# Optimization experiments

Hardware: AMD Instinct MI355X
Metric: run time of the kernel (lower is better)

## Reference

```python
import jax, jax.numpy as jnp
import numpy as np

B, N, D, H, E = 4, 1024, 512, 8, 5
HD = D // H  # head_dim = 64


def _xavier(k, shape):
    fan_out, fan_in = shape
    s = (2.0 / (fan_in + fan_out)) ** 0.5
    return jax.random.normal(k, shape, jnp.float32) * s


def setup_inputs() -> dict:
    key = jax.random.key(0)
    ks = jax.random.split(key, 7)
    x = jax.random.normal(ks[0], (B, N, D), jnp.float32)
    edge_features = jax.random.normal(ks[1], (B, N, N, E), jnp.float32)
    node_mask = jax.random.randint(ks[2], (B, N), 0, 2).astype(bool)
    w_qkv = _xavier(ks[3], (3 * D, D))
    w_ep = _xavier(ks[4], (H, E))
    w_eg = _xavier(ks[5], (H, E))
    b_eg = jnp.zeros((H,), jnp.float32)
    w_proj = _xavier(ks[6], (D, D))
    b_proj = jnp.zeros((D,), jnp.float32)
    return {"x": x, "edge_features": edge_features, "node_mask": node_mask,
            "w_qkv": w_qkv, "w_ep": w_ep, "w_eg": w_eg, "b_eg": b_eg,
            "w_proj": w_proj, "b_proj": b_proj}


def reference(x, edge_features, node_mask, w_qkv, w_ep, w_eg, b_eg, w_proj, b_proj):
    b, n, d = x.shape
    scale = HD ** -0.5
    # qkv projection (torch Linear: y = x @ W^T), split into q,k,v (b,H,n,HD)
    qkv = (x @ w_qkv.T).reshape(b, n, 3, H, HD)
    qkv = jnp.transpose(qkv, (2, 0, 3, 1, 4))
    q, k, v = qkv[0], qkv[1], qkv[2]
    # attention scores (b,H,n,n)
    scores = jnp.einsum('bhnd,bhmd->bhnm', q, k) * scale
    # edge bias and sigmoid gate, (b,n,n,E) @ (E,H) -> (b,H,n,n)
    edge_bias = jnp.einsum('bnme,he->bhnm', edge_features, w_ep)
    edge_gates = jax.nn.sigmoid(
        jnp.einsum('bnme,he->bhnm', edge_features, w_eg) + b_eg[None, :, None, None])
    scores = scores + edge_gates * edge_bias
    # pairwise valid mask, broadcast over heads
    m = node_mask[:, None, :, None] & node_mask[:, None, None, :]  # (b,1,n,n)
    scores = jnp.where(m, scores, -jnp.inf)
    row_valid = jnp.any(m, axis=-1)  # (b,1,n)
    scores = jnp.where(row_valid[..., None], scores, 0.0)
    attn = jax.nn.softmax(scores, axis=-1)
    out = jnp.einsum('bhnm,bhmd->bhnd', attn, v)
    out = jnp.transpose(out, (0, 2, 1, 3)).reshape(b, n, d)
    return out @ w_proj.T + b_proj
```

## Files before the change

kernel.cpp:

```cpp
#include <hip/hip_runtime.h>
#include <hip/hip_bf16.h>

#define Bb 4
#define Nn 1024
#define Dd 512
#define Hh 8
#define Ee 5
#define HDd 64

typedef unsigned int u32_t;
typedef unsigned short u16_t;
typedef short s16x8 __attribute__((ext_vector_type(8)));
typedef float f32x4 __attribute__((ext_vector_type(4)));

#define MFMA(a, b, c) __builtin_amdgcn_mfma_f32_16x16x32_bf16((a), (b), (c), 0, 0, 0)

__device__ __forceinline__ void lds_barrier() {
    asm volatile("s_waitcnt lgkmcnt(0)" ::: "memory");
    __builtin_amdgcn_s_barrier();
    asm volatile("" ::: "memory");
}

__device__ __forceinline__ u32_t pack32(float x) {
    u32_t u = __float_as_uint(x);
    u32_t hi = u & 0xffff0000u;
    float rem = x - __uint_as_float(hi);
    u32_t r = __float_as_uint(rem);
    u32_t lo = (r + 0x7fffu + ((r >> 16) & 1u)) >> 16;
    return hi | (lo & 0xffffu);
}

__device__ __forceinline__ void unpk8(uint4 A, uint4 B, s16x8& h, s16x8& l) {
    union { u16_t u[8]; s16x8 v; } H, L;
    u32_t a[8] = {A.x, A.y, A.z, A.w, B.x, B.y, B.z, B.w};
    #pragma unroll
    for (int i = 0; i < 8; i++) { H.u[i] = (u16_t)(a[i] >> 16); L.u[i] = (u16_t)(a[i] & 0xffffu); }
    h = H.v; l = L.v;
}

__device__ __forceinline__ void split4(uint4 A, uint2& hi, uint2& lo) {
    hi.x = (A.x >> 16) | (A.y & 0xffff0000u);
    hi.y = (A.z >> 16) | (A.w & 0xffff0000u);
    lo.x = (A.x & 0xffffu) | (A.y << 16);
    lo.y = (A.z & 0xffffu) | (A.w << 16);
}

__device__ __forceinline__ void stage16(uint4 A0, uint4 A1, uint4 A2, uint4 A3,
                                        u16_t* dh, u16_t* dl) {
    uint2 h0, l0, h1, l1, h2, l2, h3, l3;
    split4(A0, h0, l0); split4(A1, h1, l1); split4(A2, h2, l2); split4(A3, h3, l3);
    *(uint4*)(dh + 0) = make_uint4(h0.x, h0.y, h1.x, h1.y);
    *(uint4*)(dh + 8) = make_uint4(h2.x, h2.y, h3.x, h3.y);
    *(uint4*)(dl + 0) = make_uint4(l0.x, l0.y, l1.x, l1.y);
    *(uint4*)(dl + 8) = make_uint4(l2.x, l2.y, l3.x, l3.y);
}

#define HHW(a, b) (((a) >> 16) | ((b) & 0xffff0000u))
#define LLW(a, b) (((a) & 0xffffu) | ((b) << 16))

__global__ __launch_bounds__(256) void pack_prep(const float* __restrict__ x,
                                                 const float* __restrict__ wq,
                                                 const float* __restrict__ wpj,
                                                 const void* __restrict__ msk,
                                                 u32_t* __restrict__ xp,
                                                 u32_t* __restrict__ wqp,
                                                 u32_t* __restrict__ wpp,
                                                 u32_t* __restrict__ mb,
                                                 int* __restrict__ anyB) {
    __shared__ int notint;
    __shared__ int ab[Bb];
    const int tid = threadIdx.x;
    if (blockIdx.x == 1024) {
        if (tid == 0) notint = 0;
        if (tid < Bb) ab[tid] = 0;
        __syncthreads();
        const u32_t* wp = (const u32_t*)msk;
        int bad = 0;
        for (int i = tid; i < 1024; i += 256) bad |= (wp[i] > 1u);
        if (bad) atomicOr(&notint, 1);
        __syncthreads();
        const int isbyte = notint;
        const unsigned char* bp = (const unsigned char*)msk;
        if (tid < 128) {
            u32_t wbits = 0;
            for (int k = 0; k < 32; k++) {
                const int i = tid * 32 + k;
                const int v = isbyte ? (bp[i] != 0) : (wp[i] != 0);
                wbits |= (u32_t)v << k;
            }
            mb[tid] = wbits;
            if (wbits) atomicOr(&ab[tid >> 5], 1);
        }
        __syncthreads();
        if (tid < Bb) anyB[tid] = ab[tid];
        return;
    }
    const int gt = blockIdx.x * 256 + tid;
    const int gs = 1024 * 256;
    const float4* xs = (const float4*)x;
    uint4* xd = (uint4*)xp;
    for (int i = gt; i < (Bb * Nn * Dd) / 4; i += gs) {
        float4 v = xs[i];
        xd[i] = make_uint4(pack32(v.x), pack32(v.y), pack32(v.z), pack32(v.w));
    }
    const float4* qs = (const float4*)wq;
    uint4* qd = (uint4*)wqp;
    for (int i = gt; i < (3 * Dd * Dd) / 4; i += gs) {
        float4 v = qs[i];
        qd[i] = make_uint4(pack32(v.x), pack32(v.y), pack32(v.z), pack32(v.w));
    }
    const float4* ps = (const float4*)wpj;
    uint4* pd = (uint4*)wpp;
    for (int i = gt; i < (Dd * Dd) / 4; i += gs) {
        float4 v = ps[i];
        pd[i] = make_uint4(pack32(v.x), pack32(v.y), pack32(v.z), pack32(v.w));
    }
}

__global__ __launch_bounds__(256) void qkv_mfma(const u32_t* __restrict__ xp,
                                                const u32_t* __restrict__ wp,
                                                u32_t* __restrict__ q32,
                                                u32_t* __restrict__ k32,
                                                u32_t* __restrict__ v32) {
    __shared__ __align__(16) u16_t Xh[64 * 72], Xl[64 * 72];
    __shared__ __align__(16) u16_t Wh[64 * 72], Wl[64 * 72];
    const int tid = threadIdx.x;
    const int wv = tid >> 6, lane = tid & 63, lm = lane & 15, quad = lane >> 4;
    const int m0 = blockIdx.y * 64, c0 = blockIdx.x * 64;
    const int row = tid >> 2, dq = tid & 3;
    const uint4* x4 = (const uint4*)xp;
    const uint4* w4 = (const uint4*)wp;

    const size_t xb0 = (size_t)(m0 + row) * 128 + dq * 4;
    const size_t wb0 = (size_t)(c0 + row) * 128 + dq * 4;
    uint4 xa0 = x4[xb0 + 0], xa1 = x4[xb0 + 1], xa2 = x4[xb0 + 2], xa3 = x4[xb0 + 3];
    uint4 wa0 = w4[wb0 + 0], wa1 = w4[wb0 + 1], wa2 = w4[wb0 + 2], wa3 = w4[wb0 + 3];

    f32x4 acc[4];
    #pragma unroll
    for (int nt = 0; nt < 4; nt++) acc[nt] = {0.f, 0.f, 0.f, 0.f};

    for (int kt = 0; kt < 8; kt++) {
        lds_barrier();
        stage16(xa0, xa1, xa2, xa3, &Xh[row * 72 + dq * 16], &Xl[row * 72 + dq * 16]);
        stage16(wa0, wa1, wa2, wa3, &Wh[row * 72 + dq * 16], &Wl[row * 72 + dq * 16]);
        const int ktn = (kt < 7) ? kt + 1 : 7;
        xa0 = x4[xb0 + ktn * 16 + 0]; xa1 = x4[xb0 + ktn * 16 + 1];
        xa2 = x4[xb0 + ktn * 16 + 2]; xa3 = x4[xb0 + ktn * 16 + 3];
        wa0 = w4[wb0 + ktn * 16 + 0]; wa1 = w4[wb0 + ktn * 16 + 1];
        wa2 = w4[wb0 + ktn * 16 + 2]; wa3 = w4[wb0 + ktn * 16 + 3];
        lds_barrier();
        s16x8 ah[2], al[2];
        #pragma unroll
        for (int ks = 0; ks < 2; ks++) {
            ah[ks] = *(const s16x8*)&Xh[(16 * wv + lm) * 72 + ks * 32 + quad * 8];
            al[ks] = *(const s16x8*)&Xl[(16 * wv + lm) * 72 + ks * 32 + quad * 8];
        }
        #pragma unroll
        for (int nt = 0; nt < 4; nt++) {
            #pragma unroll
            for (int ks = 0; ks < 2; ks++) {
                s16x8 bh = *(const s16x8*)&Wh[(16 * nt + lm) * 72 + ks * 32 + quad * 8];
                s16x8 bl = *(const s16x8*)&Wl[(16 * nt + lm) * 72 + ks * 32 + quad * 8];
                acc[nt] = MFMA(ah[ks], bh, acc[nt]);
                acc[nt] = MFMA(ah[ks], bl, acc[nt]);
                acc[nt] = MFMA(al[ks], bh, acc[nt]);
            }
        }
    }
    #pragma unroll
    for (int nt = 0; nt < 4; nt++) {
        const int c = c0 + 16 * nt + lm;
        const int s = c >> 9, hd = c & 511, h = hd >> 6, d = hd & 63;
        u32_t* dst = (s == 0) ? q32 : (s == 1) ? k32 : v32;
        #pragma unroll
        for (int r = 0; r < 4; r++) {
            const int m = m0 + 16 * wv + 4 * quad + r;
            const int b = m >> 10, n = m & (Nn - 1);
            dst[(((size_t)b * Hh + h) * Nn + n) * HDd + d] = pack32(acc[nt][r]);
        }
    }
}

__global__ __launch_bounds__(256, 2) void attn_mfma(const u32_t* __restrict__ q32,
                                                    const u32_t* __restrict__ k32,
                                                    const u32_t* __restrict__ v32,
                                                    const float* __restrict__ ef,
                                                    const u32_t* __restrict__ mb,
                                                    const int* __restrict__ anyB,
                                                    const float* __restrict__ wep,
                                                    const float* __restrict__ weg,
                                                    const float* __restrict__ beg,
                                                    u32_t* __restrict__ aoutp) {
    __shared__ __align__(16) u16_t Kh[64 * 72], Kl[64 * 72];
    __shared__ __align__(16) u16_t VTh[64 * 88], VTl[64 * 88];
    __shared__ __align__(16) u32_t Ppk[64 * 68];

    const int tid = threadIdx.x;
    const int wv = tid >> 6, lane = tid & 63, lm = lane & 15, quad = lane >> 4;
    const int i0 = blockIdx.x * 64;
    const int h  = blockIdx.y;
    const int b  = blockIdx.z;
    const int row = tid >> 2, dq = tid & 3;
    const int jo = tid >> 5, dch = tid & 31;

    const uint4* kg4 = (const uint4*)(k32 + (((size_t)b * Hh + h) * Nn) * HDd);
    const uint2* vg2 = (const uint2*)(v32 + (((size_t)b * Hh + h) * Nn) * HDd);
    const u32_t* mbB = mb + b * 32;

    const int i_sm = i0 + 16 * wv + lm;

    const u32_t* qrow = q32 + (((size_t)b * Hh + h) * Nn + i_sm) * HDd;
    uint4 qA0 = *(const uint4*)&qrow[quad * 8];
    uint4 qB0 = *(const uint4*)&qrow[quad * 8 + 4];
    uint4 qA1 = *(const uint4*)&qrow[32 + quad * 8];
    uint4 qB1 = *(const uint4*)&qrow[32 + quad * 8 + 4];
    const size_t kb0 = (size_t)row * 16 + dq * 4;
    uint4 kr0 = kg4[kb0 + 0], kr1 = kg4[kb0 + 1], kr2 = kg4[kb0 + 2], kr3 = kg4[kb0 + 3];
    uint2 vq0 = vg2[(8 * jo + 0) * 32 + dch], vq1 = vg2[(8 * jo + 1) * 32 + dch],
          vq2 = vg2[(8 * jo + 2) * 32 + dch], vq3 = vg2[(8 * jo + 3) * 32 + dch],
          vq4 = vg2[(8 * jo + 4) * 32 + dch], vq5 = vg2[(8 * jo + 5) * 32 + dch],
          vq6 = vg2[(8 * jo + 6) * 32 + dch], vq7 = vg2[(8 * jo + 7) * 32 + dch];

    const float* efL = ef + ((size_t)(b * Nn + i_sm) * Nn + 4 * quad) * Ee;
    uint2 mwc = *(const uint2*)&mbB[0];
    float4 er4[4][5];
    #pragma unroll
    for (int jn = 0; jn < 4; jn++) {
        const float4* p4 = (const float4*)(efL + (size_t)(16 * jn) * Ee);
        #pragma unroll
        for (int c = 0; c < 5; c++) er4[jn][c] = p4[c];
    }

    const float wp0 = wep[h*Ee+0], wp1 = wep[h*Ee+1], wp2 = wep[h*Ee+2],
                wp3 = wep[h*Ee+3], wp4 = wep[h*Ee+4];
    const float wg0 = weg[h*Ee+0], wg1 = weg[h*Ee+1], wg2 = weg[h*Ee+2],
                wg3 = weg[h*Ee+3], wg4 = weg[h*Ee+4];
    const float bgs = beg[h];
    const int anyb = anyB[b];
    const int rvs = anyb && ((mbB[i_sm >> 5] >> (i_sm & 31)) & 1);

    s16x8 qh[2], ql[2];
    unpk8(qA0, qB0, qh[0], ql[0]);
    unpk8(qA1, qB1, qh[1], ql[1]);

    float m_ = -1e30f, l_ = 0.f;
    f32x4 accO[4];
    #pragma unroll
    for (int dn = 0; dn < 4; dn++) accO[dn] = {0.f, 0.f, 0.f, 0.f};
    const int xk = 8 * (lm & 3);

    for (int jt = 0; jt < Nn / 64; jt++) {
        const int jtn = (jt + 1 < Nn / 64) ? jt + 1 : Nn / 64 - 1;
        const int j0n = jtn * 64;

        lds_barrier();

        stage16(kr0, kr1, kr2, kr3, &Kh[row * 72 + dq * 16], &Kl[row * 72 + dq * 16]);
        {
            const int d0 = 2 * dch, d1 = d0 + 1;
            uint4 H0 = make_uint4(HHW(vq0.x, vq1.x), HHW(vq2.x, vq3.x),
                                  HHW(vq4.x, vq5.x), HHW(vq6.x, vq7.x));
            uint4 L0 = make_uint4(LLW(vq0.x, vq1.x), LLW(vq2.x, vq3.x),
                                  LLW(vq4.x, vq5.x), LLW(vq6.x, vq7.x));
            uint4 H1 = make_uint4(HHW(vq0.y, vq1.y), HHW(vq2.y, vq3.y),
                                  HHW(vq4.y, vq5.y), HHW(vq6.y, vq7.y));
            uint4 L1 = make_uint4(LLW(vq0.y, vq1.y), LLW(vq2.y, vq3.y),
                                  LLW(vq4.y, vq5.y), LLW(vq6.y, vq7.y));
            *(uint4*)&VTh[d0 * 88 + 8 * jo] = H0;
            *(uint4*)&VTl[d0 * 88 + 8 * jo] = L0;
            *(uint4*)&VTh[d1 * 88 + 8 * jo] = H1;
            *(uint4*)&VTl[d1 * 88 + 8 * jo] = L1;
        }
        {
            const size_t kbn = (size_t)(j0n + row) * 16 + dq * 4;
            kr0 = kg4[kbn + 0]; kr1 = kg4[kbn + 1]; kr2 = kg4[kbn + 2]; kr3 = kg4[kbn + 3];
            vq0 = vg2[(j0n + 8 * jo + 0) * 32 + dch];
            vq1 = vg2[(j0n + 8 * jo + 1) * 32 + dch];
            vq2 = vg2[(j0n + 8 * jo + 2) * 32 + dch];
            vq3 = vg2[(j0n + 8 * jo + 3) * 32 + dch];
            vq4 = vg2[(j0n + 8 * jo + 4) * 32 + dch];
            vq5 = vg2[(j0n + 8 * jo + 5) * 32 + dch];
            vq6 = vg2[(j0n + 8 * jo + 6) * 32 + dch];
            vq7 = vg2[(j0n + 8 * jo + 7) * 32 + dch];
        }

        lds_barrier();

        f32x4 Sp[4];
        #pragma unroll
        for (int jn = 0; jn < 4; jn++) {
            f32x4 s = {0.f, 0.f, 0.f, 0.f};
            #pragma unroll
            for (int ks = 0; ks < 2; ks++) {
                s16x8 kh = *(const s16x8*)&Kh[(16 * jn + lm) * 72 + ks * 32 + quad * 8];
                s16x8 kl = *(const s16x8*)&Kl[(16 * jn + lm) * 72 + ks * 32 + quad * 8];
                s = MFMA(kh, qh[ks], s);
                s = MFMA(kh, ql[ks], s);
                s = MFMA(kl, qh[ks], s);
            }
            Sp[jn] = s;
        }

        const u32_t sj0 = mwc.x >> (4 * quad), sj1 = mwc.x >> (4 * quad + 16);
        const u32_t sj2 = mwc.y >> (4 * quad), sj3 = mwc.y >> (4 * quad + 16);
        const u32_t sj[4] = {sj0, sj1, sj2, sj3};
        float pp[4][4];
        #pragma unroll
        for (int jn = 0; jn < 4; jn++) {
            #pragma unroll
            for (int r = 0; r < 4; r++) {
                const int mjv = (sj[jn] >> r) & 1;
                const int f = r * 5;
                const float e0 = er4[jn][(f+0)>>2][(f+0)&3];
                const float e1 = er4[jn][(f+1)>>2][(f+1)&3];
                const float e2 = er4[jn][(f+2)>>2][(f+2)&3];
                const float e3 = er4[jn][(f+3)>>2][(f+3)&3];
                const float e4 = er4[jn][(f+4)>>2][(f+4)&3];
                const float bias = fmaf(e0, wp0, fmaf(e1, wp1, fmaf(e2, wp2, fmaf(e3, wp3, e4 * wp4))));
                const float gv = fmaf(e0, wg0, fmaf(e1, wg1, fmaf(e2, wg2, fmaf(e3, wg3, fmaf(e4, wg4, bgs)))));
                const float gate = __builtin_amdgcn_rcpf(1.f + __expf(-gv));
                const float val = fmaf(Sp[jn][r], 0.125f, gate * bias);
                pp[jn][r] = rvs ? (mjv ? val : -1e30f) : 0.f;
            }
        }
        mwc = *(const uint2*)&mbB[j0n >> 5];
        #pragma unroll
        for (int jn = 0; jn < 4; jn++) {
            const float4* p4 = (const float4*)(efL + (size_t)(j0n + 16 * jn) * Ee);
            #pragma unroll
            for (int c = 0; c < 5; c++) er4[jn][c] = p4[c];
        }

        float tmax = fmaxf(fmaxf(fmaxf(pp[0][0], pp[0][1]), fmaxf(pp[0][2], pp[0][3])),
                           fmaxf(fmaxf(pp[1][0], pp[1][1]), fmaxf(pp[1][2], pp[1][3])));
        tmax = fmaxf(tmax,
               fmaxf(fmaxf(fmaxf(pp[2][0], pp[2][1]), fmaxf(pp[2][2], pp[2][3])),
                     fmaxf(fmaxf(pp[3][0], pp[3][1]), fmaxf(pp[3][2], pp[3][3]))));
        tmax = fmaxf(tmax, __shfl_xor(tmax, 16));
        tmax = fmaxf(tmax, __shfl_xor(tmax, 32));
        const float mnew = fmaxf(m_, tmax);
        const float alpha = __expf(m_ - mnew);
        float ps = 0.f;
        #pragma unroll
        for (int jn = 0; jn < 4; jn++)
            #pragma unroll
            for (int r = 0; r < 4; r++) { pp[jn][r] = __expf(pp[jn][r] - mnew); ps += pp[jn][r]; }
        ps += __shfl_xor(ps, 16);
        ps += __shfl_xor(ps, 32);
        m_ = mnew;
        l_ = l_ * alpha + ps;
        float a4[4];
        #pragma unroll
        for (int r = 0; r < 4; r++) a4[r] = __shfl(alpha, 4 * quad + r);
        #pragma unroll
        for (int dn = 0; dn < 4; dn++)
            #pragma unroll
            for (int r = 0; r < 4; r++) accO[dn][r] *= a4[r];

        #pragma unroll
        for (int jn = 0; jn < 4; jn++) {
            #pragma unroll
            for (int p = 0; p < 2; p++) {
                const int col = (16 * jn + 4 * quad + 2 * p) ^ xk;
                *(uint2*)&Ppk[(16 * wv + lm) * 68 + col] =
                    make_uint2(pack32(pp[jn][2 * p]), pack32(pp[jn][2 * p + 1]));
            }
        }

        s16x8 ph[2], pl[2];
        #pragma unroll
        for (int ks2 = 0; ks2 < 2; ks2++) {
            const int off = (16 * wv + lm) * 68 + ((ks2 * 32 + quad * 8) ^ xk);
            uint4 A = *(const uint4*)&Ppk[off];
            uint4 B2 = *(const uint4*)&Ppk[off + 4];
            unpk8(A, B2, ph[ks2], pl[ks2]);
        }
        #pragma unroll
        for (int dn = 0; dn < 4; dn++) {
            f32x4 c = accO[dn];
            #pragma unroll
            for (int ks2 = 0; ks2 < 2; ks2++) {
                s16x8 vh = *(const s16x8*)&VTh[(16 * dn + lm) * 88 + ks2 * 32 + quad * 8];
                s16x8 vl = *(const s16x8*)&VTl[(16 * dn + lm) * 88 + ks2 * 32 + quad * 8];
                c = MFMA(ph[ks2], vh, c);
                c = MFMA(ph[ks2], vl, c);
                c = MFMA(pl[ks2], vh, c);
            }
            accO[dn] = c;
        }
    }

    float linv[4];
    #pragma unroll
    for (int r = 0; r < 4; r++) linv[r] = __builtin_amdgcn_rcpf(__shfl(l_, 4 * quad + r));
    #pragma unroll
    for (int r = 0; r < 4; r++) {
        const int i = i0 + 16 * wv + 4 * quad + r;
        #pragma unroll
        for (int dn = 0; dn < 4; dn++)
            aoutp[(size_t)(b * Nn + i) * Dd + h * HDd + 16 * dn + lm] = pack32(accO[dn][r] * linv[r]);
    }
}

__global__ __launch_bounds__(256) void out_mfma(const u32_t* __restrict__ ap,
                                                const u32_t* __restrict__ wp,
                                                const float* __restrict__ bias,
                                                float* __restrict__ out) {
    __shared__ __align__(16) u16_t Xh[64 * 72], Xl[64 * 72];
    __shared__ __align__(16) u16_t Wh[64 * 72], Wl[64 * 72];
    const int tid = threadIdx.x;
    const int wv = tid >> 6, lane = tid & 63, lm = lane & 15, quad = lane >> 4;
    const int m0 = blockIdx.y * 64, c0 = blockIdx.x * 64;
    const int row = tid >> 2, dq = tid & 3;
    const uint4* a4 = (const uint4*)ap;
    const uint4* w4 = (const uint4*)wp;

    const size_t ab0 = (size_t)(m0 + row) * 128 + dq * 4;
    const size_t wb0 = (size_t)(c0 + row) * 128 + dq * 4;
    uint4 xa0 = a4[ab0 + 0], xa1 = a4[ab0 + 1], xa2 = a4[ab0 + 2], xa3 = a4[ab0 + 3];
    uint4 wa0 = w4[wb0 + 0], wa1 = w4[wb0 + 1], wa2 = w4[wb0 + 2], wa3 = w4[wb0 + 3];

    f32x4 acc[4];
    #pragma unroll
    for (int nt = 0; nt < 4; nt++) acc[nt] = {0.f, 0.f, 0.f, 0.f};

    for (int kt = 0; kt < 8; kt++) {
        lds_barrier();
        stage16(xa0, xa1, xa2, xa3, &Xh[row * 72 + dq * 16], &Xl[row * 72 + dq * 16]);
        stage16(wa0, wa1, wa2, wa3, &Wh[row * 72 + dq * 16], &Wl[row * 72 + dq * 16]);
        const int ktn = (kt < 7) ? kt + 1 : 7;
        xa0 = a4[ab0 + ktn * 16 + 0]; xa1 = a4[ab0 + ktn * 16 + 1];
        xa2 = a4[ab0 + ktn * 16 + 2]; xa3 = a4[ab0 + ktn * 16 + 3];
        wa0 = w4[wb0 + ktn * 16 + 0]; wa1 = w4[wb0 + ktn * 16 + 1];
        wa2 = w4[wb0 + ktn * 16 + 2]; wa3 = w4[wb0 + ktn * 16 + 3];
        lds_barrier();
        s16x8 ah[2], al[2];
        #pragma unroll
        for (int ks = 0; ks < 2; ks++) {
            ah[ks] = *(const s16x8*)&Xh[(16 * wv + lm) * 72 + ks * 32 + quad * 8];
            al[ks] = *(const s16x8*)&Xl[(16 * wv + lm) * 72 + ks * 32 + quad * 8];
        }
        #pragma unroll
        for (int nt = 0; nt < 4; nt++) {
            #pragma unroll
            for (int ks = 0; ks < 2; ks++) {
                s16x8 bh = *(const s16x8*)&Wh[(16 * nt + lm) * 72 + ks * 32 + quad * 8];
                s16x8 bl = *(const s16x8*)&Wl[(16 * nt + lm) * 72 + ks * 32 + quad * 8];
                acc[nt] = MFMA(ah[ks], bh, acc[nt]);
                acc[nt] = MFMA(ah[ks], bl, acc[nt]);
                acc[nt] = MFMA(al[ks], bh, acc[nt]);
            }
        }
    }
    #pragma unroll
    for (int nt = 0; nt < 4; nt++) {
        const int c = c0 + 16 * nt + lm;
        const float bc = bias[c];
        #pragma unroll
        for (int r = 0; r < 4; r++) {
            const int m = m0 + 16 * wv + 4 * quad + r;
            out[(size_t)m * Dd + c] = acc[nt][r] + bc;
        }
    }
}

extern "C" void kernel_launch(void* const* d_in, const int* in_sizes, int n_in,
                              void* d_out, int out_size, void* d_ws, size_t ws_size,
                              hipStream_t stream) {
    const float* x    = (const float*)d_in[0];
    const float* ef   = (const float*)d_in[1];
    const void*  msk  = d_in[2];
    const float* wqkv = (const float*)d_in[3];
    const float* wep  = (const float*)d_in[4];
    const float* weg  = (const float*)d_in[5];
    const float* beg  = (const float*)d_in[6];
    const float* wpj  = (const float*)d_in[7];
    const float* bpj  = (const float*)d_in[8];
    float* out = (float*)d_out;

    u32_t* mbits = (u32_t*)d_ws;
    int* anyB = (int*)(mbits + 128);
    u32_t* q32 = (u32_t*)(anyB + 16);
    const size_t per = (size_t)Bb * Hh * Nn * HDd;
    u32_t* k32 = q32 + per;
    u32_t* v32 = k32 + per;
    u32_t* aop = v32 + per;
    u32_t* xp  = aop + (size_t)Bb * Nn * Dd;
    u32_t* wqp = xp + (size_t)Bb * Nn * Dd;
    u32_t* wpp = wqp + (size_t)3 * Dd * Dd;

    pack_prep<<<1025, 256, 0, stream>>>(x, wqkv, wpj, msk, xp, wqp, wpp, mbits, anyB);
    qkv_mfma<<<dim3(24, 64), 256, 0, stream>>>(xp, wqp, q32, k32, v32);
    attn_mfma<<<dim3(Nn / 64, Hh, Bb), 256, 0, stream>>>(q32, k32, v32, ef, mbits, anyB,
                                                         wep, weg, beg, aop);
    out_mfma<<<dim3(8, 64), 256, 0, stream>>>(aop, wpp, bpj, out);
}
```

Before: 300.1 us.

## Split attention over key halves with combine kernel and register-shuffled P operand

Splits the attention key range into two halves per query tile, doubling the grid, and adds a combine kernel that merges the partial outputs using the saved row max and sum. The P matrix now stays in registers and is rearranged with cross-lane shuffles, replacing the LDS round trip. The MFMA operand order is swapped so the output is transposed, and the V tile uses XOR swizzling with a narrower LDS pitch. Occupancy is raised to 4 blocks per CU. The cost is an extra kernel launch, extra partial-result memory traffic, and reuse of the xp buffer for partial output.

```diff
diff --git a/kernel.cpp b/kernel.cpp
--- a/kernel.cpp
+++ b/kernel.cpp
@@ -28,6 +28,10 @@
     u32_t r = __float_as_uint(rem);
     u32_t lo = (r + 0x7fffu + ((r >> 16) & 1u)) >> 16;
     return hi | (lo & 0xffffu);
+}
+
+__device__ __forceinline__ float unpkf(u32_t x) {
+    return __uint_as_float(x & 0xffff0000u) + __uint_as_float(x << 16);
 }
 
 __device__ __forceinline__ void unpk8(uint4 A, uint4 B, s16x8& h, s16x8& l) {
@@ -182,7 +186,7 @@
     }
 }
 
-__global__ __launch_bounds__(256, 2) void attn_mfma(const u32_t* __restrict__ q32,
+__global__ __launch_bounds__(256, 4) void attn_mfma(const u32_t* __restrict__ q32,
                                                     const u32_t* __restrict__ k32,
                                                     const u32_t* __restrict__ v32,
                                                     const float* __restrict__ ef,
@@ -191,18 +195,24 @@
                                                     const float* __restrict__ wep,
                                                     const float* __restrict__ weg,
                                                     const float* __restrict__ beg,
-                                                    u32_t* __restrict__ aoutp) {
+                                                    u32_t* __restrict__ pout0,
+                                                    u32_t* __restrict__ pout1,
+                                                    float2* __restrict__ ml0,
+                                                    float2* __restrict__ ml1) {
     __shared__ __align__(16) u16_t Kh[64 * 72], Kl[64 * 72];
-    __shared__ __align__(16) u16_t VTh[64 * 88], VTl[64 * 88];
-    __shared__ __align__(16) u32_t Ppk[64 * 68];
+    __shared__ __align__(16) u16_t VTh[64 * 72], VTl[64 * 72];
 
     const int tid = threadIdx.x;
     const int wv = tid >> 6, lane = tid & 63, lm = lane & 15, quad = lane >> 4;
-    const int i0 = blockIdx.x * 64;
+    const int i0 = (blockIdx.x & 15) * 64;
+    const int half = blockIdx.x >> 4;
+    const int jbase = half * 512;
     const int h  = blockIdx.y;
     const int b  = blockIdx.z;
     const int row = tid >> 2, dq = tid & 3;
     const int jo = tid >> 5, dch = tid & 31;
+    const int wsw = 8 * ((dch >> 2) & 1);
+    const int vsw = 8 * ((lm >> 3) & 1);
 
     const uint4* kg4 = (const uint4*)(k32 + (((size_t)b * Hh + h) * Nn) * HDd);
     const uint2* vg2 = (const uint2*)(v32 + (((size_t)b * Hh + h) * Nn) * HDd);
@@ -215,19 +225,19 @@
     uint4 qB0 = *(const uint4*)&qrow[quad * 8 + 4];
     uint4 qA1 = *(const uint4*)&qrow[32 + quad * 8];
     uint4 qB1 = *(const uint4*)&qrow[32 + quad * 8 + 4];
-    const size_t kb0 = (size_t)row * 16 + dq * 4;
+    const size_t kb0 = (size_t)(jbase + row) * 16 + dq * 4;
     uint4 kr0 = kg4[kb0 + 0], kr1 = kg4[kb0 + 1], kr2 = kg4[kb0 + 2], kr3 = kg4[kb0 + 3];
-    uint2 vq0 = vg2[(8 * jo + 0) * 32 + dch], vq1 = vg2[(8 * jo + 1) * 32 + dch],
-          vq2 = vg2[(8 * jo + 2) * 32 + dch], vq3 = vg2[(8 * jo + 3) * 32 + dch],
-          vq4 = vg2[(8 * jo + 4) * 32 + dch], vq5 = vg2[(8 * jo + 5) * 32 + dch],
-          vq6 = vg2[(8 * jo + 6) * 32 + dch], vq7 = vg2[(8 * jo + 7) * 32 + dch];
+    uint2 vq0 = vg2[(jbase + 8 * jo + 0) * 32 + dch], vq1 = vg2[(jbase + 8 * jo + 1) * 32 + dch],
+          vq2 = vg2[(jbase + 8 * jo + 2) * 32 + dch], vq3 = vg2[(jbase + 8 * jo + 3) * 32 + dch],
+          vq4 = vg2[(jbase + 8 * jo + 4) * 32 + dch], vq5 = vg2[(jbase + 8 * jo + 5) * 32 + dch],
+          vq6 = vg2[(jbase + 8 * jo + 6) * 32 + dch], vq7 = vg2[(jbase + 8 * jo + 7) * 32 + dch];
 
     const float* efL = ef + ((size_t)(b * Nn + i_sm) * Nn + 4 * quad) * Ee;
-    uint2 mwc = *(const uint2*)&mbB[0];
+    uint2 mwc = *(const uint2*)&mbB[jbase >> 5];
     float4 er4[4][5];
     #pragma unroll
     for (int jn = 0; jn < 4; jn++) {
-        const float4* p4 = (const float4*)(efL + (size_t)(16 * jn) * Ee);
+        const float4* p4 = (const float4*)(efL + (size_t)(jbase + 16 * jn) * Ee);
         #pragma unroll
         for (int c = 0; c < 5; c++) er4[jn][c] = p4[c];
     }
@@ -248,17 +258,16 @@
     f32x4 accO[4];
     #pragma unroll
     for (int dn = 0; dn < 4; dn++) accO[dn] = {0.f, 0.f, 0.f, 0.f};
-    const int xk = 8 * (lm & 3);
-
-    for (int jt = 0; jt < Nn / 64; jt++) {
-        const int jtn = (jt + 1 < Nn / 64) ? jt + 1 : Nn / 64 - 1;
-        const int j0n = jtn * 64;
+
+    for (int jt = 0; jt < 8; jt++) {
+        const int j0n = jbase + ((jt < 7) ? jt + 1 : 7) * 64;
 
         lds_barrier();
 
         stage16(kr0, kr1, kr2, kr3, &Kh[row * 72 + dq * 16], &Kl[row * 72 + dq * 16]);
         {
             const int d0 = 2 * dch, d1 = d0 + 1;
+            const int jcol = (8 * jo) ^ wsw;
             uint4 H0 = make_uint4(HHW(vq0.x, vq1.x), HHW(vq2.x, vq3.x),
                                   HHW(vq4.x, vq5.x), HHW(vq6.x, vq7.x));
             uint4 L0 = make_uint4(LLW(vq0.x, vq1.x), LLW(vq2.x, vq3.x),
@@ -267,10 +276,10 @@
                                   HHW(vq4.y, vq5.y), HHW(vq6.y, vq7.y));
             uint4 L1 = make_uint4(LLW(vq0.y, vq1.y), LLW(vq2.y, vq3.y),
                                   LLW(vq4.y, vq5.y), LLW(vq6.y, vq7.y));
-            *(uint4*)&VTh[d0 * 88 + 8 * jo] = H0;
-            *(uint4*)&VTl[d0 * 88 + 8 * jo] = L0;
-            *(uint4*)&VTh[d1 * 88 + 8 * jo] = H1;
-            *(uint4*)&VTl[d1 * 88 + 8 * jo] = L1;
+            *(uint4*)&VTh[d0 * 72 + jcol] = H0;
+            *(uint4*)&VTl[d0 * 72 + jcol] = L0;
+            *(uint4*)&VTh[d1 * 72 + jcol] = H1;
+            *(uint4*)&VTl[d1 * 72 + jcol] = L1;
         }
         {
             const size_t kbn = (size_t)(j0n + row) * 16 + dq * 4;
@@ -302,9 +311,8 @@
             Sp[jn] = s;
         }
 
-        const u32_t sj0 = mwc.x >> (4 * quad), sj1 = mwc.x >> (4 * quad + 16);
-        const u32_t sj2 = mwc.y >> (4 * quad), sj3 = mwc.y >> (4 * quad + 16);
-        const u32_t sj[4] = {sj0, sj1, sj2, sj3};
+        const u32_t sj[4] = {mwc.x >> (4 * quad), mwc.x >> (4 * quad + 16),
+                             mwc.y >> (4 * quad), mwc.y >> (4 * quad + 16)};
         float pp[4][4];
         #pragma unroll
         for (int jn = 0; jn < 4; jn++) {
@@ -350,57 +358,93 @@
         ps += __shfl_xor(ps, 32);
         m_ = mnew;
         l_ = l_ * alpha + ps;
-        float a4[4];
-        #pragma unroll
-        for (int r = 0; r < 4; r++) a4[r] = __shfl(alpha, 4 * quad + r);
-        #pragma unroll
-        for (int dn = 0; dn < 4; dn++)
-            #pragma unroll
-            for (int r = 0; r < 4; r++) accO[dn][r] *= a4[r];
-
-        #pragma unroll
-        for (int jn = 0; jn < 4; jn++) {
-            #pragma unroll
-            for (int p = 0; p < 2; p++) {
-                const int col = (16 * jn + 4 * quad + 2 * p) ^ xk;
-                *(uint2*)&Ppk[(16 * wv + lm) * 68 + col] =
-                    make_uint2(pack32(pp[jn][2 * p]), pack32(pp[jn][2 * p + 1]));
-            }
-        }
-
-        s16x8 ph[2], pl[2];
-        #pragma unroll
-        for (int ks2 = 0; ks2 < 2; ks2++) {
-            const int off = (16 * wv + lm) * 68 + ((ks2 * 32 + quad * 8) ^ xk);
-            uint4 A = *(const uint4*)&Ppk[off];
-            uint4 B2 = *(const uint4*)&Ppk[off + 4];
-            unpk8(A, B2, ph[ks2], pl[ks2]);
-        }
+        #pragma unroll
+        for (int dn = 0; dn < 4; dn++) accO[dn] *= alpha;
+
+        u32_t P32[4][4];
+        #pragma unroll
+        for (int jn = 0; jn < 4; jn++)
+            #pragma unroll
+            for (int r = 0; r < 4; r++) P32[jn][r] = pack32(pp[jn][r]);
+        const bool lowpair = (quad & 2) == 0;
+        u32_t kept[8], send1[8];
+        #pragma unroll
+        for (int t = 0; t < 4; t++) {
+            kept[t]     = lowpair ? P32[0][t] : P32[1][t];
+            kept[4+t]   = lowpair ? P32[2][t] : P32[3][t];
+            send1[t]    = lowpair ? P32[1][t] : P32[0][t];
+            send1[4+t]  = lowpair ? P32[3][t] : P32[2][t];
+        }
+        u32_t R8[8], T8[8];
+        #pragma unroll
+        for (int t = 0; t < 8; t++) R8[t] = __shfl_xor((int)send1[t], 32);
+        const bool sendR = (quad == 0) || (quad == 3);
+        #pragma unroll
+        for (int t = 0; t < 8; t++) {
+            u32_t s2 = sendR ? R8[t] : kept[t];
+            T8[t] = __shfl_xor((int)s2, 16);
+        }
+        u32_t XL[8], XH[8];
+        #pragma unroll
+        for (int t = 0; t < 8; t++) {
+            XL[t] = (quad == 0) ? kept[t] : ((quad == 2) ? R8[t] : T8[t]);
+            XH[t] = (quad == 3) ? kept[t] : ((quad == 1) ? R8[t] : T8[t]);
+        }
+        s16x8 bh[2], bl[2];
+        unpk8(make_uint4(XL[0], XL[1], XL[2], XL[3]),
+              make_uint4(XH[0], XH[1], XH[2], XH[3]), bh[0], bl[0]);
+        unpk8(make_uint4(XL[4], XL[5], XL[6], XL[7]),
+              make_uint4(XH[4], XH[5], XH[6], XH[7]), bh[1], bl[1]);
+
         #pragma unroll
         for (int dn = 0; dn < 4; dn++) {
             f32x4 c = accO[dn];
             #pragma unroll
-            for (int ks2 = 0; ks2 < 2; ks2++) {
-                s16x8 vh = *(const s16x8*)&VTh[(16 * dn + lm) * 88 + ks2 * 32 + quad * 8];
-                s16x8 vl = *(const s16x8*)&VTl[(16 * dn + lm) * 88 + ks2 * 32 + quad * 8];
-                c = MFMA(ph[ks2], vh, c);
-                c = MFMA(ph[ks2], vl, c);
-                c = MFMA(pl[ks2], vh, c);
+            for (int ks = 0; ks < 2; ks++) {
+                const int off = (16 * dn + lm) * 72 + ((ks * 32 + quad * 8) ^ vsw);
+                s16x8 vh = *(const s16x8*)&VTh[off];
+                s16x8 vl = *(const s16x8*)&VTl[off];
+                c = MFMA(vh, bh[ks], c);
+                c = MFMA(vh, bl[ks], c);
+                c = MFMA(vl, bh[ks], c);
             }
             accO[dn] = c;
         }
     }
 
-    float linv[4];
-    #pragma unroll
-    for (int r = 0; r < 4; r++) linv[r] = __builtin_amdgcn_rcpf(__shfl(l_, 4 * quad + r));
-    #pragma unroll
-    for (int r = 0; r < 4; r++) {
-        const int i = i0 + 16 * wv + 4 * quad + r;
-        #pragma unroll
-        for (int dn = 0; dn < 4; dn++)
-            aoutp[(size_t)(b * Nn + i) * Dd + h * HDd + 16 * dn + lm] = pack32(accO[dn][r] * linv[r]);
-    }
+    u32_t* pout = half ? pout1 : pout0;
+    float2* mlo = half ? ml1 : ml0;
+    const size_t obase = (size_t)(b * Nn + i_sm) * Dd + h * HDd;
+    #pragma unroll
+    for (int dn = 0; dn < 4; dn++) {
+        uint4 o = make_uint4(pack32(accO[dn][0]), pack32(accO[dn][1]),
+                             pack32(accO[dn][2]), pack32(accO[dn][3]));
+        *(uint4*)&pout[obase + 16 * dn + 4 * quad] = o;
+    }
+    if (quad == 0) mlo[((size_t)b * Hh + h) * Nn + i_sm] = make_float2(m_, l_);
+}
+
+__global__ __launch_bounds__(256) void combine(const u32_t* __restrict__ p0,
+                                               const u32_t* __restrict__ p1,
+                                               const float2* __restrict__ mla,
+                                               const float2* __restrict__ mlb,
+                                               u32_t* __restrict__ aop) {
+    const int g = blockIdx.x * 256 + threadIdx.x;
+    const int rowi = g >> 4, dq = (g & 15) * 4;
+    const int b = rowi >> 13, h = (rowi >> 10) & 7, i = rowi & 1023;
+    const float2 A = mla[rowi], B = mlb[rowi];
+    const float mN = fmaxf(A.x, B.x);
+    const float a0 = __expf(A.x - mN), a1 = __expf(B.x - mN);
+    const float linv = __builtin_amdgcn_rcpf(fmaf(A.y, a0, B.y * a1));
+    const size_t base = ((size_t)(b * Nn + i)) * Dd + h * HDd + dq;
+    const uint4 u0 = *(const uint4*)&p0[base];
+    const uint4 u1 = *(const uint4*)&p1[base];
+    uint4 o;
+    o.x = pack32((unpkf(u0.x) * a0 + unpkf(u1.x) * a1) * linv);
+    o.y = pack32((unpkf(u0.y) * a0 + unpkf(u1.y) * a1) * linv);
+    o.z = pack32((unpkf(u0.z) * a0 + unpkf(u1.z) * a1) * linv);
+    o.w = pack32((unpkf(u0.w) * a0 + unpkf(u1.w) * a1) * linv);
+    *(uint4*)&aop[base] = o;
 }
 
 __global__ __launch_bounds__(256) void out_mfma(const u32_t* __restrict__ ap,
@@ -489,10 +533,15 @@
     u32_t* xp  = aop + (size_t)Bb * Nn * Dd;
     u32_t* wqp = xp + (size_t)Bb * Nn * Dd;
     u32_t* wpp = wqp + (size_t)3 * Dd * Dd;
+    u32_t* pout1 = wpp + (size_t)Dd * Dd;
+    float2* ml0 = (float2*)(pout1 + (size_t)Bb * Nn * Dd);
+    float2* ml1 = ml0 + (size_t)Bb * Hh * Nn;
+    u32_t* pout0 = xp;
 
     pack_prep<<<1025, 256, 0, stream>>>(x, wqkv, wpj, msk, xp, wqp, wpp, mbits, anyB);
     qkv_mfma<<<dim3(24, 64), 256, 0, stream>>>(xp, wqp, q32, k32, v32);
-    attn_mfma<<<dim3(Nn / 64, Hh, Bb), 256, 0, stream>>>(q32, k32, v32, ef, mbits, anyB,
-                                                         wep, weg, beg, aop);
+    attn_mfma<<<dim3(32, Hh, Bb), 256, 0, stream>>>(q32, k32, v32, ef, mbits, anyB,
+                                                    wep, weg, beg, pout0, pout1, ml0, ml1);
+    combine<<<2048, 256, 0, stream>>>(pout0, pout1, ml0, ml1, aop);
     out_mfma<<<dim3(8, 64), 256, 0, stream>>>(aop, wpp, bpj, out);
 }
```

Result: slower. 479.5 us (+59.8%).
